# Kernel tuning notes

Measured on AMD Instinct MI355X. Metric: run time of the kernel, lower is better.

Reference implementation:

```python
import jax, jax.numpy as jnp
import numpy as np

NUM_USERS = 100000
NUM_ITEMS = 50000
N = NUM_USERS + NUM_ITEMS
EMB = 64
N_LAYERS = 3
N_EDGES = 4800000
BATCH = 4096


def setup_inputs() -> dict:
    key = jax.random.key(0)
    ks = jax.random.split(key, 8)
    users = jax.random.randint(ks[0], (BATCH,), 0, NUM_USERS, dtype=jnp.int64 if jax.config.jax_enable_x64 else jnp.int32)
    pos_items = jax.random.randint(ks[1], (BATCH,), 0, NUM_ITEMS)
    neg_items = jax.random.randint(ks[2], (BATCH,), 0, NUM_ITEMS)
    adj_rows = jax.random.randint(ks[3], (N_EDGES,), 0, N)
    adj_cols = jax.random.randint(ks[4], (N_EDGES,), 0, N)
    # scale values like a degree-normalized adjacency (~1/deg) to keep magnitudes stable
    adj_vals = jax.random.uniform(ks[5], (N_EDGES,), dtype=jnp.float32) * (1.0 / 32.0)
    user_emb = jax.random.normal(ks[6], (NUM_USERS, EMB), dtype=jnp.float32) * 0.1
    item_emb = jax.random.normal(ks[7], (NUM_ITEMS, EMB), dtype=jnp.float32) * 0.1
    return {"users": users, "pos_items": pos_items, "neg_items": neg_items,
            "adj_rows": adj_rows, "adj_cols": adj_cols, "adj_vals": adj_vals,
            "user_emb": user_emb, "item_emb": item_emb}


def _spmm(rows, cols, vals, x):
    # sparse (N,N) @ dense (N,E): gather columns, scale, scatter-add to rows
    gathered = x[cols] * vals[:, None]          # [n_edges, EMB]
    return jax.ops.segment_sum(gathered, rows, num_segments=N)


def reference(users, pos_items, neg_items, adj_rows, adj_cols, adj_vals, user_emb, item_emb):
    emb = jnp.concatenate([user_emb, item_emb], axis=0)  # [N, EMB]
    acc = emb
    cur = emb
    for _ in range(N_LAYERS):
        cur = _spmm(adj_rows, adj_cols, adj_vals, cur)
        acc = acc + cur
    final = acc / (N_LAYERS + 1)                # layer-wise mean
    users_emb = final[:NUM_USERS]
    items_emb = final[NUM_USERS:]
    u = users_emb[users]                        # [B, EMB]
    pos = items_emb[pos_items]
    neg = items_emb[neg_items]
    pos_scores = jnp.sum(u * pos, axis=1)       # [B]
    neg_scores = jnp.sum(u * neg, axis=1)
    return (pos_scores, neg_scores)
```

## Files before the change

### kernel.cpp

```cpp
#include <hip/hip_runtime.h>

#define NUM_USERS 100000
#define NUM_ITEMS 50000
#define NNODES    150000
#define EMB       64
#define NEDGES    4800000
#define BATCH     4096
#define BUCKETS   293
#define BROWS     512
#define EPB       8192
#define NBLK_A    586
#define CAP       17408
#define NSAMP     (3 * BATCH)

typedef unsigned short u16;
typedef unsigned int   u32;

__device__ inline float bf2f(u16 u) { return __uint_as_float(((u32)u) << 16); }
__device__ inline u16 f2bf(float f) {
    u32 b = __float_as_uint(f);
    b += 0x7FFFu + ((b >> 16) & 1u);
    return (u16)(b >> 16);
}
__device__ inline u32 pack2(float a, float b) {
    return (u32)f2bf(a) | ((u32)f2bf(b) << 16);
}

__global__ void init_kernel(const float* __restrict__ user_emb,
                            const float* __restrict__ item_emb,
                            u16* __restrict__ l0) {
    long i = (long)blockIdx.x * blockDim.x + threadIdx.x;
    const long n4 = (long)NNODES * EMB / 4;
    if (i >= n4) return;
    const long nu4 = (long)NUM_USERS * EMB / 4;
    float4 v = (i < nu4) ? ((const float4*)user_emb)[i]
                         : ((const float4*)item_emb)[i - nu4];
    ushort4 o;
    o.x = f2bf(v.x); o.y = f2bf(v.y); o.z = f2bf(v.z); o.w = f2bf(v.w);
    ((ushort4*)l0)[i] = o;
}

__global__ void __launch_bounds__(512) binA_kernel(const int* __restrict__ rows,
                                                   const int* __restrict__ cols,
                                                   const float* __restrict__ vals,
                                                   int* __restrict__ bfill,
                                                   int2* __restrict__ tmp) {
    __shared__ int2 ebuf[EPB];
    __shared__ int  hist[BUCKETS];
    __shared__ int  start[BUCKETS];
    __shared__ int  cursor[BUCKETS];
    __shared__ int  gbase[BUCKETS];
    const int tid = threadIdx.x;
    for (int i = tid; i < BUCKETS; i += 512) hist[i] = 0;
    __syncthreads();

    const long base = (long)blockIdx.x * EPB;
    int rsave[16];
    #pragma unroll
    for (int k = 0; k < 16; ++k) {
        long e = base + (long)k * 512 + tid;
        int r = -1;
        if (e < NEDGES) {
            r = rows[e];
            atomicAdd(&hist[r >> 9], 1);
        }
        rsave[k] = r;
    }
    __syncthreads();

    if (tid < 64) {
        int carry = 0;
        for (int cb = 0; cb < BUCKETS; cb += 64) {
            int i = cb + tid;
            int orig = (i < BUCKETS) ? hist[i] : 0;
            int x = orig;
            #pragma unroll
            for (int d = 1; d < 64; d <<= 1) {
                int t = __shfl_up(x, d, 64);
                if (tid >= d) x += t;
            }
            int total = __shfl(x, 63, 64);
            if (i < BUCKETS) { start[i] = x - orig + carry; cursor[i] = x - orig + carry; }
            carry += total;
        }
    }
    __syncthreads();

    for (int b = tid; b < BUCKETS; b += 512) {
        int h = hist[b];
        gbase[b] = h ? b * CAP + atomicAdd(&bfill[b], h) : 0;
    }

    #pragma unroll
    for (int k = 0; k < 16; ++k) {
        int r = rsave[k];
        if (r >= 0) {
            long e = base + (long)k * 512 + tid;
            int pos = atomicAdd(&cursor[r >> 9], 1);
            ebuf[pos] = make_int2(((r & 511) << 18) | cols[e], __float_as_int(vals[e]));
        }
    }
    __syncthreads();

    const int wv = tid >> 6, lane = tid & 63;
    const int* eb32 = (const int*)ebuf;
    int* gtmp = (int*)tmp;
    for (int b = wv; b < BUCKETS; b += 8) {
        int cnt2 = hist[b] * 2;
        if (!cnt2) continue;
        int  s2 = start[b] * 2;
        long d2 = (long)gbase[b] * 2;
        for (int i = lane; i < cnt2; i += 64)
            gtmp[d2 + i] = eb32[s2 + i];
    }
}

__global__ void scan_buckets(const int* __restrict__ bfill, int* __restrict__ bucketBase) {
    int lane = threadIdx.x;
    int carry = 0;
    for (int cb = 0; cb < BUCKETS; cb += 64) {
        int i = cb + lane;
        int orig = (i < BUCKETS) ? bfill[i] : 0;
        int x = orig;
        #pragma unroll
        for (int d = 1; d < 64; d <<= 1) {
            int t = __shfl_up(x, d, 64);
            if (lane >= d) x += t;
        }
        int total = __shfl(x, 63, 64);
        if (i < BUCKETS) bucketBase[i] = x - orig + carry;
        carry += total;
    }
}

__global__ void __launch_bounds__(512) binB_kernel(const int* __restrict__ bfill,
                                                   const int* __restrict__ bucketBase,
                                                   const int2* __restrict__ tmp,
                                                   int* __restrict__ rowPtr,
                                                   int2* __restrict__ csr) {
    const int bucket = blockIdx.x;
    __shared__ int lhist[BROWS];
    __shared__ int rp[BROWS];
    __shared__ int fill[BROWS];
    const int t = threadIdx.x;
    lhist[t] = 0; fill[t] = 0;
    __syncthreads();

    const int cnt = bfill[bucket];
    const int2* src = tmp + (long)bucket * CAP;
    for (int k = t; k < cnt; k += 512)
        atomicAdd(&lhist[src[k].x >> 18], 1);
    __syncthreads();

    const int gb = bucketBase[bucket];
    if (t < 64) {
        int carry = 0;
        for (int cb = 0; cb < BROWS; cb += 64) {
            int i = cb + t;
            int orig = lhist[i];
            int x = orig;
            #pragma unroll
            for (int d = 1; d < 64; d <<= 1) {
                int tt = __shfl_up(x, d, 64);
                if (t >= d) x += tt;
            }
            int total = __shfl(x, 63, 64);
            rp[i] = x - orig + carry + gb;
            carry += total;
        }
    }
    __syncthreads();

    int rowIdx = bucket * BROWS + t;
    rowPtr[rowIdx] = rp[t];

    for (int k = t; k < cnt; k += 512) {
        int2 p = src[k];
        int rL = p.x >> 18;
        int pos = rp[rL] + atomicAdd(&fill[rL], 1);
        csr[pos] = make_int2(p.x & 0x3FFFF, p.y);
    }
}

#define ACCX(V, X) { \
    a[0] += (V) * __uint_as_float((X).x << 16); \
    a[1] += (V) * __uint_as_float((X).x & 0xFFFF0000u); \
    a[2] += (V) * __uint_as_float((X).y << 16); \
    a[3] += (V) * __uint_as_float((X).y & 0xFFFF0000u); \
    a[4] += (V) * __uint_as_float((X).z << 16); \
    a[5] += (V) * __uint_as_float((X).z & 0xFFFF0000u); \
    a[6] += (V) * __uint_as_float((X).w << 16); \
    a[7] += (V) * __uint_as_float((X).w & 0xFFFF0000u); }

__global__ void spmm_csr(const int* __restrict__ rowPtr, const int2* __restrict__ csr,
                         const u16* __restrict__ cur, u16* __restrict__ nxt) {
    int gtid = blockIdx.x * blockDim.x + threadIdx.x;
    int row = gtid >> 3;
    int t   = gtid & 7;
    if (row >= NNODES) return;
    int beg = rowPtr[row], end = rowPtr[row + 1];
    float a[8];
    #pragma unroll
    for (int i = 0; i < 8; ++i) a[i] = 0.f;

    int e = beg;
    for (; e + 7 < end; e += 8) {
        int2 p[8];
        #pragma unroll
        for (int j = 0; j < 8; ++j) p[j] = csr[e + j];
        uint4 x[8];
        #pragma unroll
        for (int j = 0; j < 8; ++j)
            x[j] = *(const uint4*)(cur + ((long)p[j].x << 6) + (t << 3));
        #pragma unroll
        for (int j = 0; j < 8; ++j) {
            float v = __int_as_float(p[j].y);
            ACCX(v, x[j]);
        }
    }
    for (; e < end; ++e) {
        int2 p = csr[e];
        float v = __int_as_float(p.y);
        uint4 x = *(const uint4*)(cur + ((long)p.x << 6) + (t << 3));
        ACCX(v, x);
    }

    uint4 o;
    o.x = pack2(a[0], a[1]);
    o.y = pack2(a[2], a[3]);
    o.z = pack2(a[4], a[5]);
    o.w = pack2(a[6], a[7]);
    *(uint4*)(nxt + ((long)row << 6) + (t << 3)) = o;
}

__global__ void spmm_sampled(const int* __restrict__ users,
                             const int* __restrict__ pos_items,
                             const int* __restrict__ neg_items,
                             const int* __restrict__ rowPtr, const int2* __restrict__ csr,
                             const u16* __restrict__ cur, float* __restrict__ sampled) {
    int gtid = blockIdx.x * blockDim.x + threadIdx.x;
    int slot = gtid >> 3;
    int t    = gtid & 7;
    if (slot >= NSAMP) return;
    int row;
    if (slot < BATCH)          row = users[slot];
    else if (slot < 2 * BATCH) row = pos_items[slot - BATCH] + NUM_USERS;
    else                       row = neg_items[slot - 2 * BATCH] + NUM_USERS;

    int beg = rowPtr[row], end = rowPtr[row + 1];
    float a[8];
    #pragma unroll
    for (int i = 0; i < 8; ++i) a[i] = 0.f;

    int e = beg;
    for (; e + 7 < end; e += 8) {
        int2 p[8];
        #pragma unroll
        for (int j = 0; j < 8; ++j) p[j] = csr[e + j];
        uint4 x[8];
        #pragma unroll
        for (int j = 0; j < 8; ++j)
            x[j] = *(const uint4*)(cur + ((long)p[j].x << 6) + (t << 3));
        #pragma unroll
        for (int j = 0; j < 8; ++j) {
            float v = __int_as_float(p[j].y);
            ACCX(v, x[j]);
        }
    }
    for (; e < end; ++e) {
        int2 p = csr[e];
        float v = __int_as_float(p.y);
        uint4 x = *(const uint4*)(cur + ((long)p.x << 6) + (t << 3));
        ACCX(v, x);
    }

    float4* dst = (float4*)(sampled + ((long)slot << 6) + (t << 3));
    dst[0] = make_float4(a[0], a[1], a[2], a[3]);
    dst[1] = make_float4(a[4], a[5], a[6], a[7]);
}

__global__ void score_kernel(const int* __restrict__ users,
                             const int* __restrict__ pos_items,
                             const int* __restrict__ neg_items,
                             const float* __restrict__ uemb,
                             const float* __restrict__ iemb,
                             const u16* __restrict__ l1,
                             const u16* __restrict__ l2,
                             const float* __restrict__ sampled,
                             float* __restrict__ out) {
    int gtid = blockIdx.x * blockDim.x + threadIdx.x;
    int wave = gtid >> 6;
    int lane = threadIdx.x & 63;
    if (wave >= BATCH) return;
    int u = users[wave];
    int p = pos_items[wave];
    int n = neg_items[wave];
    long U = (long)u * EMB + lane;
    long P = (long)(p + NUM_USERS) * EMB + lane;
    long N = (long)(n + NUM_USERS) * EMB + lane;
    float ue = uemb[(long)u * EMB + lane] + bf2f(l1[U]) + bf2f(l2[U])
             + sampled[(long)wave * EMB + lane];
    float pe = iemb[(long)p * EMB + lane] + bf2f(l1[P]) + bf2f(l2[P])
             + sampled[(long)(BATCH + wave) * EMB + lane];
    float ne = iemb[(long)n * EMB + lane] + bf2f(l1[N]) + bf2f(l2[N])
             + sampled[(long)(2 * BATCH + wave) * EMB + lane];
    float ps = ue * pe;
    float ns = ue * ne;
    #pragma unroll
    for (int off = 32; off > 0; off >>= 1) {
        ps += __shfl_down(ps, off, 64);
        ns += __shfl_down(ns, off, 64);
    }
    if (lane == 0) {
        out[wave]         = ps * 0.0625f;
        out[BATCH + wave] = ns * 0.0625f;
    }
}

extern "C" void kernel_launch(void* const* d_in, const int* in_sizes, int n_in,
                              void* d_out, int out_size, void* d_ws, size_t ws_size,
                              hipStream_t stream) {
    const int*   users = (const int*)d_in[0];
    const int*   pos   = (const int*)d_in[1];
    const int*   neg   = (const int*)d_in[2];
    const int*   rows  = (const int*)d_in[3];
    const int*   cols  = (const int*)d_in[4];
    const float* vals  = (const float*)d_in[5];
    const float* uemb  = (const float*)d_in[6];
    const float* iemb  = (const float*)d_in[7];
    float* out = (float*)d_out;

    const size_t tblElems = (size_t)NNODES * EMB;
    u16*  B0      = (u16*)d_ws;
    u16*  B1      = B0 + tblElems;
    u16*  B2      = B1 + tblElems;
    int2* tmp     = (int2*)(B2 + tblElems);
    int2* csr     = (int2*)(tmp + (size_t)BUCKETS * CAP);
    int*  rowPtr  = (int*)(csr + NEDGES);
    int*  bfill   = rowPtr + 150016;
    int*  bucketB = bfill + 320;
    float* sampled= (float*)(bucketB + 320);

    hipMemsetAsync(bfill, 0, 320 * sizeof(int), stream);

    binA_kernel<<<NBLK_A, 512, 0, stream>>>(rows, cols, vals, bfill, tmp);
    scan_buckets<<<1, 64, 0, stream>>>(bfill, bucketB);
    binB_kernel<<<BUCKETS, 512, 0, stream>>>(bfill, bucketB, tmp, rowPtr, csr);

    const long n4 = (long)tblElems / 4;
    init_kernel<<<(int)((n4 + 255) / 256), 256, 0, stream>>>(uemb, iemb, B0);

    const long nth = (long)NNODES * 8;
    const int  spmmGrid = (int)((nth + 255) / 256);
    spmm_csr<<<spmmGrid, 256, 0, stream>>>(rowPtr, csr, B0, B1);
    spmm_csr<<<spmmGrid, 256, 0, stream>>>(rowPtr, csr, B1, B2);
    spmm_sampled<<<(NSAMP * 8 + 255) / 256, 256, 0, stream>>>(users, pos, neg,
                                                              rowPtr, csr, B2, sampled);

    score_kernel<<<(BATCH * 64) / 256, 256, 0, stream>>>(users, pos, neg,
                                                         uemb, iemb, B1, B2, sampled, out);
}
```

Before: 456.3 us.

## Software-pipeline SpMM gathers, fold bucket scan into binB, add nontemporal accesses

The SpMM row loop becomes a double-buffered pipeline: the next 8 edges are loaded and their embedding rows gathered while the previous batch is accumulated, and the scalar tail is replaced by one masked batch of 8. The separate scan_buckets launch is removed; each binB block computes its global base by reducing bfill over all earlier buckets. Streaming reads and writes of edges, embeddings and outputs use nontemporal builtins, the binA copy-out moves to 64-bit words, and launch bounds of (256,4) are added. The double buffers raise register pressure, and the per-block prefix reduction repeats work across blocks.

```diff
diff --git a/kernel.cpp b/kernel.cpp
--- a/kernel.cpp
+++ b/kernel.cpp
@@ -15,6 +15,9 @@
 
 typedef unsigned short u16;
 typedef unsigned int   u32;
+typedef unsigned long long u64;
+typedef float f32x4 __attribute__((ext_vector_type(4)));
+typedef u32   u32x4 __attribute__((ext_vector_type(4)));
 
 __device__ inline float bf2f(u16 u) { return __uint_as_float(((u32)u) << 16); }
 __device__ inline u16 f2bf(float f) {
@@ -33,8 +36,9 @@
     const long n4 = (long)NNODES * EMB / 4;
     if (i >= n4) return;
     const long nu4 = (long)NUM_USERS * EMB / 4;
-    float4 v = (i < nu4) ? ((const float4*)user_emb)[i]
-                         : ((const float4*)item_emb)[i - nu4];
+    f32x4 v;
+    if (i < nu4) v = __builtin_nontemporal_load((const f32x4*)user_emb + i);
+    else         v = __builtin_nontemporal_load((const f32x4*)item_emb + (i - nu4));
     ushort4 o;
     o.x = f2bf(v.x); o.y = f2bf(v.y); o.z = f2bf(v.z); o.w = f2bf(v.w);
     ((ushort4*)l0)[i] = o;
@@ -61,7 +65,7 @@
         long e = base + (long)k * 512 + tid;
         int r = -1;
         if (e < NEDGES) {
-            r = rows[e];
+            r = __builtin_nontemporal_load(rows + e);
             atomicAdd(&hist[r >> 9], 1);
         }
         rsave[k] = r;
@@ -97,44 +101,27 @@
         if (r >= 0) {
             long e = base + (long)k * 512 + tid;
             int pos = atomicAdd(&cursor[r >> 9], 1);
-            ebuf[pos] = make_int2(((r & 511) << 18) | cols[e], __float_as_int(vals[e]));
+            int c = __builtin_nontemporal_load(cols + e);
+            float v = __builtin_nontemporal_load(vals + e);
+            ebuf[pos] = make_int2(((r & 511) << 18) | c, __float_as_int(v));
         }
     }
     __syncthreads();
 
     const int wv = tid >> 6, lane = tid & 63;
-    const int* eb32 = (const int*)ebuf;
-    int* gtmp = (int*)tmp;
+    const u64* eb8 = (const u64*)ebuf;
+    u64* gt8 = (u64*)tmp;
     for (int b = wv; b < BUCKETS; b += 8) {
-        int cnt2 = hist[b] * 2;
-        if (!cnt2) continue;
-        int  s2 = start[b] * 2;
-        long d2 = (long)gbase[b] * 2;
-        for (int i = lane; i < cnt2; i += 64)
-            gtmp[d2 + i] = eb32[s2 + i];
-    }
-}
-
-__global__ void scan_buckets(const int* __restrict__ bfill, int* __restrict__ bucketBase) {
-    int lane = threadIdx.x;
-    int carry = 0;
-    for (int cb = 0; cb < BUCKETS; cb += 64) {
-        int i = cb + lane;
-        int orig = (i < BUCKETS) ? bfill[i] : 0;
-        int x = orig;
-        #pragma unroll
-        for (int d = 1; d < 64; d <<= 1) {
-            int t = __shfl_up(x, d, 64);
-            if (lane >= d) x += t;
-        }
-        int total = __shfl(x, 63, 64);
-        if (i < BUCKETS) bucketBase[i] = x - orig + carry;
-        carry += total;
+        int cnt = hist[b];
+        if (!cnt) continue;
+        int  s = start[b];
+        long d = (long)gbase[b];
+        for (int i = lane; i < cnt; i += 64)
+            __builtin_nontemporal_store(eb8[s + i], gt8 + d + i);
     }
 }
 
 __global__ void __launch_bounds__(512) binB_kernel(const int* __restrict__ bfill,
-                                                   const int* __restrict__ bucketBase,
                                                    const int2* __restrict__ tmp,
                                                    int* __restrict__ rowPtr,
                                                    int2* __restrict__ csr) {
@@ -152,8 +139,13 @@
         atomicAdd(&lhist[src[k].x >> 18], 1);
     __syncthreads();
 
-    const int gb = bucketBase[bucket];
     if (t < 64) {
+        int s = 0;
+        for (int i = t; i < bucket; i += 64) s += bfill[i];
+        #pragma unroll
+        for (int off = 32; off > 0; off >>= 1) s += __shfl_down(s, off, 64);
+        int gb = __shfl(s, 0, 64);
+
         int carry = 0;
         for (int cb = 0; cb < BROWS; cb += 64) {
             int i = cb + t;
@@ -192,8 +184,63 @@
     a[6] += (V) * __uint_as_float((X).w << 16); \
     a[7] += (V) * __uint_as_float((X).w & 0xFFFF0000u); }
 
-__global__ void spmm_csr(const int* __restrict__ rowPtr, const int2* __restrict__ csr,
-                         const u16* __restrict__ cur, u16* __restrict__ nxt) {
+__device__ __forceinline__ void row_accum(int beg, int end, int t,
+                                          const int2* __restrict__ csr,
+                                          const u16* __restrict__ cur,
+                                          float* __restrict__ a) {
+    int len = end - beg;
+    int nfull = len >> 3;
+    uint4 xA[8], xB[8];
+    float vA[8], vB[8];
+    int2  pA[8], pB[8];
+
+#define LOADP(P, E) { _Pragma("unroll") \
+    for (int j = 0; j < 8; ++j) P[j] = csr[(E) + j]; }
+#define GATH(X, V, P) { _Pragma("unroll") \
+    for (int j = 0; j < 8; ++j) { \
+        X[j] = *(const uint4*)(cur + ((long)P[j].x << 6) + (t << 3)); \
+        V[j] = __int_as_float(P[j].y); } }
+#define ACC8(X, V) { _Pragma("unroll") \
+    for (int j = 0; j < 8; ++j) { float vv = V[j]; ACCX(vv, X[j]); } }
+
+    if (nfull) {
+        int ge = beg;
+        LOADP(pA, ge); GATH(xA, vA, pA); ge += 8;
+        int rem = nfull - 1;
+        while (rem >= 2) {
+            LOADP(pB, ge); ACC8(xA, vA); GATH(xB, vB, pB); ge += 8;
+            LOADP(pA, ge); ACC8(xB, vB); GATH(xA, vA, pA); ge += 8;
+            rem -= 2;
+        }
+        if (rem) {
+            LOADP(pB, ge); ACC8(xA, vA); GATH(xB, vB, pB);
+            ACC8(xB, vB);
+        } else {
+            ACC8(xA, vA);
+        }
+    }
+    int e2 = beg + (nfull << 3);
+    int ntail = end - e2;
+    if (ntail) {
+        #pragma unroll
+        for (int j = 0; j < 8; ++j) {
+            int idx = e2 + j;
+            bool ok = idx < end;
+            int2 pp = csr[ok ? idx : (end - 1)];
+            if (!ok) pp.y = 0;
+            pA[j] = pp;
+        }
+        GATH(xA, vA, pA);
+        ACC8(xA, vA);
+    }
+#undef LOADP
+#undef GATH
+#undef ACC8
+}
+
+__global__ void __launch_bounds__(256, 4)
+spmm_csr(const int* __restrict__ rowPtr, const int2* __restrict__ csr,
+         const u16* __restrict__ cur, u16* __restrict__ nxt) {
     int gtid = blockIdx.x * blockDim.x + threadIdx.x;
     int row = gtid >> 3;
     int t   = gtid & 7;
@@ -203,41 +250,22 @@
     #pragma unroll
     for (int i = 0; i < 8; ++i) a[i] = 0.f;
 
-    int e = beg;
-    for (; e + 7 < end; e += 8) {
-        int2 p[8];
-        #pragma unroll
-        for (int j = 0; j < 8; ++j) p[j] = csr[e + j];
-        uint4 x[8];
-        #pragma unroll
-        for (int j = 0; j < 8; ++j)
-            x[j] = *(const uint4*)(cur + ((long)p[j].x << 6) + (t << 3));
-        #pragma unroll
-        for (int j = 0; j < 8; ++j) {
-            float v = __int_as_float(p[j].y);
-            ACCX(v, x[j]);
-        }
-    }
-    for (; e < end; ++e) {
-        int2 p = csr[e];
-        float v = __int_as_float(p.y);
-        uint4 x = *(const uint4*)(cur + ((long)p.x << 6) + (t << 3));
-        ACCX(v, x);
-    }
-
-    uint4 o;
+    row_accum(beg, end, t, csr, cur, a);
+
+    u32x4 o;
     o.x = pack2(a[0], a[1]);
     o.y = pack2(a[2], a[3]);
     o.z = pack2(a[4], a[5]);
     o.w = pack2(a[6], a[7]);
-    *(uint4*)(nxt + ((long)row << 6) + (t << 3)) = o;
-}
-
-__global__ void spmm_sampled(const int* __restrict__ users,
-                             const int* __restrict__ pos_items,
-                             const int* __restrict__ neg_items,
-                             const int* __restrict__ rowPtr, const int2* __restrict__ csr,
-                             const u16* __restrict__ cur, float* __restrict__ sampled) {
+    __builtin_nontemporal_store(o, (u32x4*)(nxt + ((long)row << 6) + (t << 3)));
+}
+
+__global__ void __launch_bounds__(256, 4)
+spmm_sampled(const int* __restrict__ users,
+             const int* __restrict__ pos_items,
+             const int* __restrict__ neg_items,
+             const int* __restrict__ rowPtr, const int2* __restrict__ csr,
+             const u16* __restrict__ cur, float* __restrict__ sampled) {
     int gtid = blockIdx.x * blockDim.x + threadIdx.x;
     int slot = gtid >> 3;
     int t    = gtid & 7;
@@ -252,27 +280,7 @@
     #pragma unroll
     for (int i = 0; i < 8; ++i) a[i] = 0.f;
 
-    int e = beg;
-    for (; e + 7 < end; e += 8) {
-        int2 p[8];
-        #pragma unroll
-        for (int j = 0; j < 8; ++j) p[j] = csr[e + j];
-        uint4 x[8];
-        #pragma unroll
-        for (int j = 0; j < 8; ++j)
-            x[j] = *(const uint4*)(cur + ((long)p[j].x << 6) + (t << 3));
-        #pragma unroll
-        for (int j = 0; j < 8; ++j) {
-            float v = __int_as_float(p[j].y);
-            ACCX(v, x[j]);
-        }
-    }
-    for (; e < end; ++e) {
-        int2 p = csr[e];
-        float v = __int_as_float(p.y);
-        uint4 x = *(const uint4*)(cur + ((long)p.x << 6) + (t << 3));
-        ACCX(v, x);
-    }
+    row_accum(beg, end, t, csr, cur, a);
 
     float4* dst = (float4*)(sampled + ((long)slot << 6) + (t << 3));
     dst[0] = make_float4(a[0], a[1], a[2], a[3]);
@@ -338,14 +346,12 @@
     int2* csr     = (int2*)(tmp + (size_t)BUCKETS * CAP);
     int*  rowPtr  = (int*)(csr + NEDGES);
     int*  bfill   = rowPtr + 150016;
-    int*  bucketB = bfill + 320;
-    float* sampled= (float*)(bucketB + 320);
+    float* sampled= (float*)(bfill + 320);
 
     hipMemsetAsync(bfill, 0, 320 * sizeof(int), stream);
 
     binA_kernel<<<NBLK_A, 512, 0, stream>>>(rows, cols, vals, bfill, tmp);
-    scan_buckets<<<1, 64, 0, stream>>>(bfill, bucketB);
-    binB_kernel<<<BUCKETS, 512, 0, stream>>>(bfill, bucketB, tmp, rowPtr, csr);
+    binB_kernel<<<BUCKETS, 512, 0, stream>>>(bfill, tmp, rowPtr, csr);
 
     const long n4 = (long)tblElems / 4;
     init_kernel<<<(int)((n4 + 255) / 256), 256, 0, stream>>>(uemb, iemb, B0);
```

Result: slower. 521.2 us (+14.2%).
